# Optimization experiments

Measured on AMD Instinct MI355X. Metric: run time of the kernel, lower is better.

## Reference

```python
import jax, jax.numpy as jnp
import numpy as np

NEG_INF = -9e15  # matches -9000000000000000.0 in the torch source


def setup_inputs() -> dict:
    key = jax.random.key(0)
    k1, k2, k3, k4 = jax.random.split(key, 4)
    B, H, N, D = 4, 8, 2048, 64
    queries = jax.random.normal(k1, (B, H, N, D), dtype=jnp.float32)
    keys = jax.random.normal(k2, (B, H, N, D), dtype=jnp.float32)
    values = jax.random.normal(k3, (B, H, N, D), dtype=jnp.float32)
    adj = jax.random.randint(k4, (N, N), 0, 2, dtype=jnp.int32)
    return {"queries": queries, "keys": keys, "values": values, "adj": adj}


def reference(queries, keys, values, adj):
    B, H, N, D = queries.shape
    # e = Q K^T / 8  (hard-coded divisor == sqrt(64))
    e = jnp.einsum("bhnd,bhmd->bhnm", queries, keys) / 8.0
    # graph-adjacency mask (adj [N,N] broadcasts over batch and heads)
    att = jnp.where(adj > 0, e, NEG_INF)
    att = jax.nn.softmax(att, axis=-1)
    # dropout p=0.0 / eval mode -> identity
    h_prime = jnp.einsum("bhnm,bhmd->bhnd", att, values)  # [B,H,N,D]
    # original uses .view (flat reshape), NOT a permute
    return h_prime.reshape(N, B, H, D)
```

## Files before the change

### kernel.cpp

```cpp
#include <hip/hip_runtime.h>
#include <math.h>

typedef short short8 __attribute__((ext_vector_type(8)));
typedef float float4_t __attribute__((ext_vector_type(4)));
typedef unsigned uint2_t __attribute__((ext_vector_type(2)));
typedef unsigned short ushort_t;

#define BH   32
#define N_   2048
#define D_   64
#define NCH  32
#define LDP  72
#define KV_ELEMS (BH * N_ * D_)
#define OFF_VF  (KV_ELEMS * 2)
#define OFF_MSK (KV_ELEMS * 4)
#define QSCALE 0.18033688f

__device__ __forceinline__ unsigned pack_bf16(float a, float b) {
  union { float f; unsigned u; } ua{a}, ub{b};
  return __builtin_amdgcn_perm(ub.u + 0x8000u, ua.u + 0x8000u, 0x07060302u);
}

__device__ __forceinline__ void gload_lds16(const ushort_t* g, ushort_t* l) {
  __builtin_amdgcn_global_load_lds(
      (const __attribute__((address_space(1))) unsigned int*)(g),
      (__attribute__((address_space(3))) unsigned int*)(l), 16, 0, 0);
}

__global__ __launch_bounds__(256) void prep_kernel(
    const float* __restrict__ K, const float* __restrict__ V,
    const int* __restrict__ adj, ushort_t* __restrict__ Kf,
    ushort_t* __restrict__ Vf, unsigned long long* __restrict__ msk) {
  __shared__ __align__(16) float Tc[64 * 68];
  const int blk = blockIdx.x, t = threadIdx.x;

  if (blk < 2048) {
    const bool isK = blk < 1024;
    const int b = isK ? blk : blk - 1024;
    const float* src = (isK ? K : V) + (b >> 5) * (N_ * D_) + (b & 31) * 64 * D_;
#pragma unroll
    for (int i = 0; i < 4; ++i) {
      int idx = i * 256 + t;
      int row = idx >> 4, c4 = (idx & 15) * 4;
      *(float4_t*)&Tc[row * 68 + c4] = *(const float4_t*)(src + row * D_ + c4);
    }
    __syncthreads();
    ushort_t* dst = (isK ? Kf : Vf) + b * 4096;
#pragma unroll
    for (int e = 0; e < 2; ++e) {
      int u = t * 2 + e;
      int g = u >> 6, lane = u & 63;
      int ks = g >> 2, quad = lane >> 4, l16 = lane & 15;
      float v[8];
      if (isK) {
        int nt = g & 3;
        const float* rp = &Tc[(nt * 16 + l16) * 68 + ks * 32 + quad * 8];
        float4_t a = *(const float4_t*)(rp);
        float4_t bq = *(const float4_t*)(rp + 4);
#pragma unroll
        for (int j = 0; j < 4; ++j) { v[j] = a[j]; v[4 + j] = bq[j]; }
      } else {
        int dt = g & 3, d = dt * 16 + l16;
#pragma unroll
        for (int j = 0; j < 8; ++j) {
          int key = 16 * (j & 3) + ks * 8 + quad * 2 + (j >> 2);
          v[j] = Tc[key * 68 + d];
        }
      }
      union { short8 s; unsigned u4[4]; } h;
      h.u4[0] = pack_bf16(v[0], v[1]); h.u4[1] = pack_bf16(v[2], v[3]);
      h.u4[2] = pack_bf16(v[4], v[5]); h.u4[3] = pack_bf16(v[6], v[7]);
      *(short8*)(dst + u * 8) = h.s;
    }
  } else {
    const int row = (blk - 2048) * 4 + (t >> 6);
    const int lane = t & 63;
    unsigned long long keep = 0;
#pragma unroll 8
    for (int i = 0; i < 32; ++i) {
      int a = adj[row * N_ + i * 64 + lane];
      unsigned long long b = __ballot(a > 0);
      if (lane == i) keep = b;
    }
    if (lane < 32) msk[row * 32 + lane] = keep;
  }
}

__global__ __launch_bounds__(512) void attn_main(
    const float* __restrict__ Q, const ushort_t* __restrict__ Kf,
    const ushort_t* __restrict__ Vf, const unsigned long long* __restrict__ msk,
    float* __restrict__ O) {
  __shared__ __align__(16) ushort_t kv[2][8192];
  __shared__ __align__(16) ushort_t lds_p[8][16 * LDP];

  const int t    = threadIdx.x;
  const int w    = t >> 6;
  const int lane = t & 63;
  const int quad = lane >> 4;
  const int l16  = lane & 15;
  const int bh   = blockIdx.x & (BH - 1);
  const int qt   = blockIdx.x >> 5;
  const int base = bh * (N_ * D_);
  const int qrow0 = qt * 128 + w * 16;

  const ushort_t* Kfb = Kf + (bh * 32) * 4096;
  const ushort_t* Vfb = Vf + (bh * 32) * 4096;
  const unsigned long long* mr = msk + (qrow0 + quad * 4) * 32;

  short8 qf[2];
#pragma unroll
  for (int ks = 0; ks < 2; ++ks) {
    const float* qp = Q + base + (qrow0 + l16) * D_ + ks * 32 + quad * 8;
    float4_t f0 = *(const float4_t*)(qp);
    float4_t f1 = *(const float4_t*)(qp + 4);
    union { short8 s; unsigned u[4]; } h;
    h.u[0] = pack_bf16(f0[0] * QSCALE, f0[1] * QSCALE);
    h.u[1] = pack_bf16(f0[2] * QSCALE, f0[3] * QSCALE);
    h.u[2] = pack_bf16(f1[0] * QSCALE, f1[1] * QSCALE);
    h.u[3] = pack_bf16(f1[2] * QSCALE, f1[3] * QSCALE);
    qf[ks] = h.s;
  }

  short8 ones;
#pragma unroll
  for (int j = 0; j < 8; ++j) ones[j] = (short)0x3F80;

  float4_t oacc[4];
  float4_t osum;
#pragma unroll
  for (int dt = 0; dt < 4; ++dt) oacc[dt] = (float4_t){0.f, 0.f, 0.f, 0.f};
  osum = (float4_t){0.f, 0.f, 0.f, 0.f};

  const int fo = lane * 8;

#define STAGE(nb, c)                                                          \
  do {                                                                        \
    const ushort_t* _s = (w < 4 ? Kfb + (c)*4096 + w * 1024                   \
                                : Vfb + (c)*4096 + (w - 4) * 1024) + lane * 8;\
    ushort_t* _d = &kv[nb][w * 1024];                                         \
    gload_lds16(_s, _d);                                                      \
    gload_lds16(_s + 512, _d + 512);                                          \
  } while (0)

  STAGE(0, 0);

#pragma unroll 2
  for (int c = 0; c < NCH; ++c) {
    const int cur = c & 1;
    __syncthreads();

    unsigned long long mw[4];
#pragma unroll
    for (int r = 0; r < 4; ++r) mw[r] = mr[r * 32 + c];

    if (c + 1 < NCH) STAGE(cur ^ 1, c + 1);

    const ushort_t* kb = &kv[cur][0];
    const ushort_t* vb = &kv[cur][4096];

    float4_t sacc[4];
#pragma unroll
    for (int nt = 0; nt < 4; ++nt) sacc[nt] = (float4_t){0.f, 0.f, 0.f, 0.f};
#pragma unroll
    for (int ks = 0; ks < 2; ++ks)
#pragma unroll
      for (int nt = 0; nt < 4; ++nt) {
        short8 kfr = *(const short8*)(kb + (ks * 4 + nt) * 512 + fo);
        sacc[nt] = __builtin_amdgcn_mfma_f32_16x16x32_bf16(qf[ks], kfr, sacc[nt], 0, 0, 0);
      }

#pragma unroll
    for (int r = 0; r < 4; ++r) {
      unsigned long long sh = mw[r] >> l16;
      unsigned lo = (unsigned)sh, hi = (unsigned)(sh >> 32);
      float p0 = (lo & 1u)       ? exp2f(sacc[0][r]) : 0.f;
      float p1 = (lo & 0x10000u) ? exp2f(sacc[1][r]) : 0.f;
      float p2 = (hi & 1u)       ? exp2f(sacc[2][r]) : 0.f;
      float p3 = (hi & 0x10000u) ? exp2f(sacc[3][r]) : 0.f;
      uint2_t d2;
      d2.x = pack_bf16(p0, p1);
      d2.y = pack_bf16(p2, p3);
      *(uint2_t*)&lds_p[w][(quad * 4 + r) * LDP + (l16 << 2)] = d2;
    }

#pragma unroll
    for (int ks = 0; ks < 2; ++ks) {
      short8 pf = *(const short8*)&lds_p[w][l16 * LDP + ks * 32 + quad * 8];
#pragma unroll
      for (int dt = 0; dt < 4; ++dt) {
        short8 vfr = *(const short8*)(vb + (ks * 4 + dt) * 512 + fo);
        oacc[dt] = __builtin_amdgcn_mfma_f32_16x16x32_bf16(pf, vfr, oacc[dt], 0, 0, 0);
      }
      osum = __builtin_amdgcn_mfma_f32_16x16x32_bf16(pf, ones, osum, 0, 0, 0);
    }
  }

#pragma unroll
  for (int r = 0; r < 4; ++r) {
    float inv = 1.f / osum[r];
    int qi = qrow0 + quad * 4 + r;
#pragma unroll
    for (int dt = 0; dt < 4; ++dt)
      O[base + qi * D_ + dt * 16 + l16] = oacc[dt][r] * inv;
  }
}

extern "C" void kernel_launch(void* const* d_in, const int* in_sizes, int n_in,
                              void* d_out, int out_size, void* d_ws, size_t ws_size,
                              hipStream_t stream) {
  const float* Q  = (const float*)d_in[0];
  const float* K  = (const float*)d_in[1];
  const float* V  = (const float*)d_in[2];
  const int* adj  = (const int*)d_in[3];
  float* O        = (float*)d_out;
  ushort_t* Kf    = (ushort_t*)d_ws;
  ushort_t* Vf    = (ushort_t*)((char*)d_ws + OFF_VF);
  unsigned long long* msk = (unsigned long long*)((char*)d_ws + OFF_MSK);

  prep_kernel<<<2560, 256, 0, stream>>>(K, V, adj, Kf, Vf, msk);
  attn_main<<<512, 512, 0, stream>>>(Q, Kf, Vf, msk, O);
}
```

Before: 170.8 us.

## Switch attention to 32x32x16 MFMA with key-split wave pairs and register P

Rewrites the main attention loop to use 32x32x16 bf16 MFMAs computing S^T (K as A operand). The transposed layout lets the exp'd probabilities feed the PV MFMA directly from registers, removing the per-wave LDS round trip for P. Each pair of waves splits every 64-key chunk in half, and the partial O and row sums are combined through shared memory at the end. The row sum is now accumulated in scalar registers instead of through an extra MFMA against a ones vector. The prep kernel re-lays out K/V fragments and transposes the mask for the new access pattern, and launch bounds now request 4 blocks, which adds register pressure risk.

Result: faster. 154.2 us (-9.7%).

```diff
diff --git a/kernel.cpp b/kernel.cpp
--- a/kernel.cpp
+++ b/kernel.cpp
@@ -3,14 +3,13 @@
 
 typedef short short8 __attribute__((ext_vector_type(8)));
 typedef float float4_t __attribute__((ext_vector_type(4)));
-typedef unsigned uint2_t __attribute__((ext_vector_type(2)));
+typedef float f32x16 __attribute__((ext_vector_type(16)));
 typedef unsigned short ushort_t;
 
 #define BH   32
 #define N_   2048
 #define D_   64
 #define NCH  32
-#define LDP  72
 #define KV_ELEMS (BH * N_ * D_)
 #define OFF_VF  (KV_ELEMS * 2)
 #define OFF_MSK (KV_ELEMS * 4)
@@ -50,21 +49,21 @@
     for (int e = 0; e < 2; ++e) {
       int u = t * 2 + e;
       int g = u >> 6, lane = u & 63;
-      int ks = g >> 2, quad = lane >> 4, l16 = lane & 15;
+      int hi = lane >> 5, l32 = lane & 31;
       float v[8];
       if (isK) {
-        int nt = g & 3;
-        const float* rp = &Tc[(nt * 16 + l16) * 68 + ks * 32 + quad * 8];
+        int nt = g >> 2, ks = g & 3;
+        const float* rp = &Tc[(nt * 32 + l32) * 68 + ks * 16 + hi * 8];
         float4_t a = *(const float4_t*)(rp);
         float4_t bq = *(const float4_t*)(rp + 4);
 #pragma unroll
         for (int j = 0; j < 4; ++j) { v[j] = a[j]; v[4 + j] = bq[j]; }
       } else {
-        int dt = g & 3, d = dt * 16 + l16;
+        int nt = g >> 2, dt = (g >> 1) & 1, ksp = g & 1;
 #pragma unroll
         for (int j = 0; j < 8; ++j) {
-          int key = 16 * (j & 3) + ks * 8 + quad * 2 + (j >> 2);
-          v[j] = Tc[key * 68 + d];
+          int key = (ksp * 2 + (j >> 2)) * 8 + hi * 4 + (j & 3);
+          v[j] = Tc[(nt * 32 + key) * 68 + dt * 32 + l32];
         }
       }
       union { short8 s; unsigned u4[4]; } h;
@@ -82,35 +81,37 @@
       unsigned long long b = __ballot(a > 0);
       if (lane == i) keep = b;
     }
-    if (lane < 32) msk[row * 32 + lane] = keep;
-  }
-}
-
-__global__ __launch_bounds__(512) void attn_main(
+    if (lane < 32) msk[(size_t)lane * 2048 + row] = keep;
+  }
+}
+
+__global__ __launch_bounds__(512, 4) void attn_main(
     const float* __restrict__ Q, const ushort_t* __restrict__ Kf,
     const ushort_t* __restrict__ Vf, const unsigned long long* __restrict__ msk,
     float* __restrict__ O) {
   __shared__ __align__(16) ushort_t kv[2][8192];
-  __shared__ __align__(16) ushort_t lds_p[8][16 * LDP];
+  __shared__ float xbuf[4][17][64];
 
   const int t    = threadIdx.x;
   const int w    = t >> 6;
   const int lane = t & 63;
-  const int quad = lane >> 4;
-  const int l16  = lane & 15;
+  const int l32  = lane & 31;
+  const int hi   = lane >> 5;
+  const int pair = w >> 1;
+  const int nt   = w & 1;
   const int bh   = blockIdx.x & (BH - 1);
   const int qt   = blockIdx.x >> 5;
   const int base = bh * (N_ * D_);
-  const int qrow0 = qt * 128 + w * 16;
+  const int trow0 = qt * 128 + pair * 32;
 
   const ushort_t* Kfb = Kf + (bh * 32) * 4096;
   const ushort_t* Vfb = Vf + (bh * 32) * 4096;
-  const unsigned long long* mr = msk + (qrow0 + quad * 4) * 32;
-
-  short8 qf[2];
-#pragma unroll
-  for (int ks = 0; ks < 2; ++ks) {
-    const float* qp = Q + base + (qrow0 + l16) * D_ + ks * 32 + quad * 8;
+  const unsigned long long* mrow = msk + (trow0 + l32);
+
+  short8 qf[4];
+#pragma unroll
+  for (int ks = 0; ks < 4; ++ks) {
+    const float* qp = Q + base + (trow0 + l32) * D_ + ks * 16 + hi * 8;
     float4_t f0 = *(const float4_t*)(qp);
     float4_t f1 = *(const float4_t*)(qp + 4);
     union { short8 s; unsigned u[4]; } h;
@@ -121,15 +122,10 @@
     qf[ks] = h.s;
   }
 
-  short8 ones;
-#pragma unroll
-  for (int j = 0; j < 8; ++j) ones[j] = (short)0x3F80;
-
-  float4_t oacc[4];
-  float4_t osum;
-#pragma unroll
-  for (int dt = 0; dt < 4; ++dt) oacc[dt] = (float4_t){0.f, 0.f, 0.f, 0.f};
-  osum = (float4_t){0.f, 0.f, 0.f, 0.f};
+  f32x16 oacc0, oacc1;
+  float osum = 0.f;
+#pragma unroll
+  for (int i = 0; i < 16; ++i) { oacc0[i] = 0.f; oacc1[i] = 0.f; }
 
   const int fo = lane * 8;
 
@@ -149,59 +145,87 @@
     const int cur = c & 1;
     __syncthreads();
 
-    unsigned long long mw[4];
-#pragma unroll
-    for (int r = 0; r < 4; ++r) mw[r] = mr[r * 32 + c];
+    unsigned long long mw = mrow[(size_t)c * 2048];
 
     if (c + 1 < NCH) STAGE(cur ^ 1, c + 1);
 
     const ushort_t* kb = &kv[cur][0];
     const ushort_t* vb = &kv[cur][4096];
 
-    float4_t sacc[4];
-#pragma unroll
-    for (int nt = 0; nt < 4; ++nt) sacc[nt] = (float4_t){0.f, 0.f, 0.f, 0.f};
-#pragma unroll
-    for (int ks = 0; ks < 2; ++ks)
-#pragma unroll
-      for (int nt = 0; nt < 4; ++nt) {
-        short8 kfr = *(const short8*)(kb + (ks * 4 + nt) * 512 + fo);
-        sacc[nt] = __builtin_amdgcn_mfma_f32_16x16x32_bf16(qf[ks], kfr, sacc[nt], 0, 0, 0);
-      }
-
-#pragma unroll
-    for (int r = 0; r < 4; ++r) {
-      unsigned long long sh = mw[r] >> l16;
-      unsigned lo = (unsigned)sh, hi = (unsigned)(sh >> 32);
-      float p0 = (lo & 1u)       ? exp2f(sacc[0][r]) : 0.f;
-      float p1 = (lo & 0x10000u) ? exp2f(sacc[1][r]) : 0.f;
-      float p2 = (hi & 1u)       ? exp2f(sacc[2][r]) : 0.f;
-      float p3 = (hi & 0x10000u) ? exp2f(sacc[3][r]) : 0.f;
-      uint2_t d2;
-      d2.x = pack_bf16(p0, p1);
-      d2.y = pack_bf16(p2, p3);
-      *(uint2_t*)&lds_p[w][(quad * 4 + r) * LDP + (l16 << 2)] = d2;
-    }
-
-#pragma unroll
-    for (int ks = 0; ks < 2; ++ks) {
-      short8 pf = *(const short8*)&lds_p[w][l16 * LDP + ks * 32 + quad * 8];
-#pragma unroll
-      for (int dt = 0; dt < 4; ++dt) {
-        short8 vfr = *(const short8*)(vb + (ks * 4 + dt) * 512 + fo);
-        oacc[dt] = __builtin_amdgcn_mfma_f32_16x16x32_bf16(pf, vfr, oacc[dt], 0, 0, 0);
-      }
-      osum = __builtin_amdgcn_mfma_f32_16x16x32_bf16(pf, ones, osum, 0, 0, 0);
-    }
-  }
-
-#pragma unroll
-  for (int r = 0; r < 4; ++r) {
-    float inv = 1.f / osum[r];
-    int qi = qrow0 + quad * 4 + r;
-#pragma unroll
-    for (int dt = 0; dt < 4; ++dt)
-      O[base + qi * D_ + dt * 16 + l16] = oacc[dt][r] * inv;
+    f32x16 sacc;
+#pragma unroll
+    for (int i = 0; i < 16; ++i) sacc[i] = 0.f;
+#pragma unroll
+    for (int ks = 0; ks < 4; ++ks) {
+      short8 kfr = *(const short8*)(kb + (nt * 4 + ks) * 512 + fo);
+      sacc = __builtin_amdgcn_mfma_f32_32x32x16_bf16(kfr, qf[ks], sacc, 0, 0, 0);
+    }
+
+    unsigned half = (unsigned)(nt ? (mw >> 32) : mw);
+    half >>= (hi << 2);
+    float p[16];
+#pragma unroll
+    for (int reg = 0; reg < 16; ++reg) {
+      const int pos = (reg & 3) + 8 * (reg >> 2);
+      int sm = ((int)(half << (31 - pos))) >> 31;
+      union { float f; unsigned u; } e;
+      e.f = __builtin_amdgcn_exp2f(sacc[reg]);
+      e.u &= (unsigned)sm;
+      p[reg] = e.f;
+      osum += e.f;
+    }
+
+    union { short8 s; unsigned u[4]; } pa0, pa1;
+#pragma unroll
+    for (int jj = 0; jj < 4; ++jj) {
+      int r = (jj >> 1) * 4 + (jj & 1) * 2;
+      pa0.u[jj] = pack_bf16(p[r], p[r + 1]);
+      pa1.u[jj] = pack_bf16(p[8 + r], p[8 + r + 1]);
+    }
+
+    {
+      short8 v00 = *(const short8*)(vb + (nt * 4 + 0) * 512 + fo);
+      short8 v01 = *(const short8*)(vb + (nt * 4 + 1) * 512 + fo);
+      short8 v10 = *(const short8*)(vb + (nt * 4 + 2) * 512 + fo);
+      short8 v11 = *(const short8*)(vb + (nt * 4 + 3) * 512 + fo);
+      oacc0 = __builtin_amdgcn_mfma_f32_32x32x16_bf16(pa0.s, v00, oacc0, 0, 0, 0);
+      oacc0 = __builtin_amdgcn_mfma_f32_32x32x16_bf16(pa1.s, v01, oacc0, 0, 0, 0);
+      oacc1 = __builtin_amdgcn_mfma_f32_32x32x16_bf16(pa0.s, v10, oacc1, 0, 0, 0);
+      oacc1 = __builtin_amdgcn_mfma_f32_32x32x16_bf16(pa1.s, v11, oacc1, 0, 0, 0);
+    }
+  }
+
+  osum += __shfl_xor(osum, 32);
+
+  __syncthreads();
+  if (nt) {
+#pragma unroll
+    for (int reg = 0; reg < 16; ++reg) xbuf[pair][reg][lane] = oacc0[reg];
+    xbuf[pair][16][lane] = osum;
+  }
+  __syncthreads();
+  float inv = 0.f;
+  if (!nt) {
+    inv = 1.f / (osum + xbuf[pair][16][lane]);
+#pragma unroll
+    for (int reg = 0; reg < 16; ++reg) oacc0[reg] += xbuf[pair][reg][lane];
+  }
+  __syncthreads();
+  if (nt) {
+#pragma unroll
+    for (int reg = 0; reg < 16; ++reg) xbuf[pair][reg][lane] = oacc1[reg];
+  }
+  __syncthreads();
+  if (!nt) {
+#pragma unroll
+    for (int reg = 0; reg < 16; ++reg) {
+      int qo = (reg & 3) + 8 * (reg >> 2) + 4 * hi;
+      float iv = __shfl(inv, qo);
+      float o0 = (oacc0[reg]) * iv;
+      float o1 = (oacc1[reg] + xbuf[pair][reg][lane]) * iv;
+      O[base + (trow0 + qo) * D_ + l32]      = o0;
+      O[base + (trow0 + qo) * D_ + 32 + l32] = o1;
+    }
   }
 }
 
```
